# Kernel optimization log

Measured on AMD Instinct MI355X. Metric: run time of the kernel, lower is better.

Reference implementation:

```python
import jax, jax.numpy as jnp
import numpy as np

B, C, H, W = 2, 128, 64, 64
D_STATE, D_CONV, EXPAND = 16, 4, 2
D_INNER = EXPAND * C
DT_RANK = (C + 15) // 16  # ceil(d_model/16) = 8


def layernorm(x, w, b):
    # WithBias_LayerNorm over last (channel) dim, unbiased=False variance
    mu = jnp.mean(x, axis=-1, keepdims=True)
    var = jnp.mean((x - mu) ** 2, axis=-1, keepdims=True)
    return (x - mu) / jnp.sqrt(var + 1e-5) * w + b


def causal_conv1d_silu(x, w, b):
    # x: (b, d, l); w: (d, k) depthwise; causal pad k-1 on left, then SiLU
    k = w.shape[1]
    out = jax.lax.conv_general_dilated(
        x, w[:, None, :], window_strides=(1,), padding=[(k - 1, 0)],
        dimension_numbers=('NCH', 'OIH', 'NCH'), feature_group_count=w.shape[0])
    return jax.nn.silu(out + b[:, None])


def selective_scan(dA, dBu, Cm):
    # dA, dBu: (b, d, l, n); Cm: (b, n, l) -> y: (b, d, l)
    dA_t = jnp.moveaxis(dA, 2, 0)    # (l, b, d, n)
    dBu_t = jnp.moveaxis(dBu, 2, 0)  # (l, b, d, n)
    C_t = jnp.moveaxis(Cm, 2, 0)     # (l, b, n)

    def step(h, inp):
        a, bu, c = inp
        h = a * h + bu
        y = jnp.einsum('bdn,bn->bd', h, c)
        return h, y

    h0 = jnp.zeros(dA.shape[:2] + (dA.shape[3],), dA.dtype)
    _, ys = jax.lax.scan(step, h0, (dA_t, dBu_t, C_t))
    return jnp.moveaxis(ys, 0, 2)  # (b, d, l)


def mamba_branch(x3, W_in, W_z, conv_w, conv_b, W_x, W_dt, b_dt, A, D, W_out):
    # x3: (b, l, d_model) normalized input
    x = jnp.einsum('bld,ed->bel', x3, W_in)  # (b, d_inner, l)
    z = jnp.einsum('bld,ed->bel', x3, W_z)
    x = causal_conv1d_silu(x, conv_w, conv_b)
    xdbl = jnp.einsum('bdl,ed->bel', x, W_x)  # (b, dt_rank+2n, l)
    dt_low = xdbl[:, :DT_RANK]
    Bm = xdbl[:, DT_RANK:DT_RANK + D_STATE]
    Cm = xdbl[:, DT_RANK + D_STATE:]
    delta = jax.nn.softplus(jnp.einsum('brl,dr->bdl', dt_low, W_dt) + b_dt[:, None])
    dA = jnp.exp(delta[:, :, :, None] * A[None, :, None, :])           # (b,d,l,n)
    dBu = jnp.einsum('bdl,bnl->bdln', delta * x, Bm)                    # (b,d,l,n)
    y = selective_scan(dA, dBu, Cm)
    y = y + D[:, None] * x
    y = y * jax.nn.silu(z)
    return jnp.einsum('bdl,od->blo', y, W_out)  # (b, l, d_model)


def setup_inputs() -> dict:
    key = jax.random.key(0)
    ks = jax.random.split(key, 24)
    rn = lambda k, shp, s: jax.random.normal(k, shp, dtype=jnp.float32) * s
    inp = {}
    inp['pan'] = rn(ks[0], (B, C, H, W), 1.0)
    inp['ms'] = rn(ks[1], (B, C, H, W), 1.0)
    inp['norm_w_pan'] = jnp.ones((C,), jnp.float32)
    inp['norm_b_pan'] = jnp.zeros((C,), jnp.float32)
    inp['norm_w_ms'] = jnp.ones((C,), jnp.float32)
    inp['norm_b_ms'] = jnp.zeros((C,), jnp.float32)
    inp['W_in_pan'] = rn(ks[2], (D_INNER, C), C ** -0.5)
    inp['W_in_ms'] = rn(ks[3], (D_INNER, C), C ** -0.5)
    inp['W_z_pan'] = rn(ks[4], (D_INNER, C), C ** -0.5)
    inp['W_z_ms'] = rn(ks[5], (D_INNER, C), C ** -0.5)
    inp['conv_w_pan'] = rn(ks[6], (D_INNER, D_CONV), D_CONV ** -0.5)
    inp['conv_b_pan'] = rn(ks[7], (D_INNER,), 0.02)
    inp['conv_w_ms'] = rn(ks[8], (D_INNER, D_CONV), D_CONV ** -0.5)
    inp['conv_b_ms'] = rn(ks[9], (D_INNER,), 0.02)
    inp['W_x_pan'] = rn(ks[10], (DT_RANK + 2 * D_STATE, D_INNER), D_INNER ** -0.5)
    inp['W_x_ms'] = rn(ks[11], (DT_RANK + 2 * D_STATE, D_INNER), D_INNER ** -0.5)
    dt_std = DT_RANK ** -0.5
    inp['W_dt_pan'] = jax.random.uniform(ks[12], (D_INNER, DT_RANK), jnp.float32, -dt_std, dt_std)
    inp['W_dt_ms'] = jax.random.uniform(ks[13], (D_INNER, DT_RANK), jnp.float32, -dt_std, dt_std)
    # dt bias init: inverse-softplus of dt ~ logU[1e-3, 1e-1]
    u = np.asarray(jax.random.uniform(ks[14], (D_INNER,)))
    dt = np.exp(u * (np.log(0.1) - np.log(0.001)) + np.log(0.001)).clip(min=1e-4)
    inv_dt = dt + np.log(-np.expm1(-dt))
    inp['b_dt_pan'] = jnp.asarray(inv_dt, jnp.float32)
    inp['b_dt_ms'] = jnp.asarray(inv_dt, jnp.float32)
    inp['A_log'] = jnp.log(jnp.broadcast_to(jnp.arange(1, D_STATE + 1, dtype=jnp.float32), (D_INNER, D_STATE)))
    inp['D_pan'] = jnp.ones((D_INNER,), jnp.float32)
    inp['D_ms'] = jnp.ones((D_INNER,), jnp.float32)
    inp['W_out_pan'] = rn(ks[15], (C, D_INNER), D_INNER ** -0.5)
    inp['W_out_ms'] = rn(ks[16], (C, D_INNER), D_INNER ** -0.5)
    return inp


def reference(pan, ms, norm_w_pan, norm_b_pan, norm_w_ms, norm_b_ms,
              W_in_pan, W_in_ms, W_z_pan, W_z_ms,
              conv_w_pan, conv_b_pan, conv_w_ms, conv_b_ms,
              W_x_pan, W_x_ms, W_dt_pan, W_dt_ms, b_dt_pan, b_dt_ms,
              A_log, D_pan, D_ms, W_out_pan, W_out_ms):
    b, c, h, w = pan.shape
    A = -jnp.exp(A_log)
    pan3 = layernorm(pan.reshape(b, c, h * w).transpose(0, 2, 1), norm_w_pan, norm_b_pan)
    ms3 = layernorm(ms.reshape(b, c, h * w).transpose(0, 2, 1), norm_w_ms, norm_b_ms)
    out_pan = mamba_branch(pan3, W_in_pan, W_z_pan, conv_w_pan, conv_b_pan,
                           W_x_pan, W_dt_pan, b_dt_pan, A, D_pan, W_out_pan)
    out_ms = mamba_branch(ms3, W_in_ms, W_z_ms, conv_w_ms, conv_b_ms,
                          W_x_ms, W_dt_ms, b_dt_ms, A, D_ms, W_out_ms)
    out_pan = out_pan.transpose(0, 2, 1).reshape(b, c, h, w)
    out_ms = out_ms.transpose(0, 2, 1).reshape(b, c, h, w)
    return (out_pan, out_ms)
```

## Files before the change

### kernel.cpp

```cpp
#include <hip/hip_runtime.h>
#include <hip/hip_bf16.h>

constexpr int BB = 2;
constexpr int CC = 128;
constexpr int LL = 4096;
constexpr int DI = 256;
constexpr int DS = 16;
constexpr int DR = 8;
constexpr int DX = 40;
constexpr int NZ = 2 * BB;
constexpr int CH = 8;
constexpr int NCH = LL / CH;
constexpr int SEG = 32;

typedef short bf16x8 __attribute__((ext_vector_type(8)));
typedef float f32x4 __attribute__((ext_vector_type(4)));
typedef float f32x2 __attribute__((ext_vector_type(2)));

__device__ __forceinline__ unsigned short f2bf(float x) {
    __hip_bfloat16 h = __float2bfloat16(x);
    return *(unsigned short*)&h;
}
__device__ __forceinline__ float bflo(unsigned u) { return __uint_as_float(u << 16); }
__device__ __forceinline__ float bfhi(unsigned u) { return __uint_as_float(u & 0xffff0000u); }
__device__ __forceinline__ float bfu(unsigned short u) { return __uint_as_float((unsigned)u << 16); }
__device__ __forceinline__ float fast_rcp(float x) { return __builtin_amdgcn_rcpf(x); }
__device__ __forceinline__ float siluf(float x) { return x * fast_rcp(1.f + __expf(-x)); }
__device__ __forceinline__ float softplusf(float x) {
    const float z = exp2f(x * 1.44269504f);
    return (x > 20.f) ? x : 0.69314718f * log2f(1.f + z);
}

__global__ __launch_bounds__(256) void prep_kernel(
    const float* __restrict__ pan, const float* __restrict__ ms,
    const float* __restrict__ wpan, const float* __restrict__ bpan,
    const float* __restrict__ wms, const float* __restrict__ bms,
    const float* __restrict__ Winp, const float* __restrict__ Winm,
    const float* __restrict__ Wzp, const float* __restrict__ Wzm,
    const float* __restrict__ Woutp, const float* __restrict__ Woutm,
    const float* __restrict__ Wxp, const float* __restrict__ Wxm,
    unsigned short* __restrict__ x3b, unsigned short* __restrict__ wb)
{
    const int bx = blockIdx.x;
    const int t = threadIdx.x;
    if (bx >= 256) {
        const int i = (bx - 256) * 256 + t;
        const float* src; int off;
        if (i < 32768)       { src = Winp;  off = i; }
        else if (i < 65536)  { src = Winm;  off = i - 32768; }
        else if (i < 98304)  { src = Wzp;   off = i - 65536; }
        else if (i < 131072) { src = Wzm;   off = i - 98304; }
        else if (i < 163840) { src = Woutp; off = i - 131072; }
        else if (i < 196608) { src = Woutm; off = i - 163840; }
        else if (i < 206848) { src = Wxp;   off = i - 196608; }
        else                 { src = Wxm;   off = i - 206848; }
        wb[i] = f2bf(src[off]);
        return;
    }
    const int zi = bx >> 6;
    const int br = zi >> 1, b = zi & 1;
    const float* inp = br ? ms : pan;
    const float* wp = br ? wms : wpan;
    const float* bp = br ? bms : bpan;
    const int l0 = (bx & 63) * 64;
    const int lo = t & 63, c4 = t >> 6;
    const float* base = inp + (size_t)b * CC * LL + l0 + lo;
    float vals[32];
    float s = 0.f, s2 = 0.f;
    #pragma unroll
    for (int i = 0; i < 32; i++) {
        const int c = c4 * 32 + i;
        const float v = base[(size_t)c * LL];
        vals[i] = v; s += v; s2 += v * v;
    }
    __shared__ float red[2][4][64];
    red[0][c4][lo] = s; red[1][c4][lo] = s2;
    __syncthreads();
    const float S  = red[0][0][lo] + red[0][1][lo] + red[0][2][lo] + red[0][3][lo];
    const float S2 = red[1][0][lo] + red[1][1][lo] + red[1][2][lo] + red[1][3][lo];
    const float mu = S * (1.f / CC);
    const float var = S2 * (1.f / CC) - mu * mu;
    const float rstd = rsqrtf(var + 1e-5f);
    unsigned short* out = x3b + (size_t)zi * CC * LL + l0 + lo;
    #pragma unroll
    for (int i = 0; i < 32; i++) {
        const int c = c4 * 32 + i;
        out[(size_t)c * LL] = f2bf((vals[i] - mu) * rstd * wp[c] + bp[c]);
    }
}

__global__ __launch_bounds__(256) void gemm_inz_mfma(
    const unsigned short* __restrict__ wb, const unsigned short* __restrict__ x3b,
    unsigned short* __restrict__ xpre16, unsigned short* __restrict__ zb16)
{
    const int zi = blockIdx.z;
    const int my = blockIdx.y;
    const unsigned short* WI = wb + (zi >= BB ? 32768 : 0);
    const unsigned short* WZ = WI + 65536;
    const int mbase = my * 64;
    const unsigned short* Xb = x3b + (size_t)zi * CC * LL;
    const int n0 = blockIdx.x * 64;
    const int t = threadIdx.x;
    const int w = t >> 6, ln = t & 63;
    const int nf = ln & 15, qb = ln >> 4;
    bf16x8 afragI[4], afragZ[4];
    const int mrow = mbase + w * 16 + nf;
    #pragma unroll
    for (int c = 0; c < 4; c++) {
        afragI[c] = *(const bf16x8*)(WI + (size_t)mrow * CC + c * 32 + qb * 8);
        afragZ[c] = *(const bf16x8*)(WZ + (size_t)mrow * CC + c * 32 + qb * 8);
    }
    __shared__ unsigned short Bs[64][40];
    unsigned* Bw = (unsigned*)Bs;
    f32x4 accI[4] = {}, accZ[4] = {};
    const int kp = t >> 4, n4 = (t & 15) * 4;
    ushort4 a0 = *(const ushort4*)(Xb + (size_t)(2 * kp) * LL + n0 + n4);
    ushort4 a1 = *(const ushort4*)(Xb + (size_t)(2 * kp + 1) * LL + n0 + n4);
    #pragma unroll
    for (int kc = 0; kc < 4; kc++) {
        if (kc) __syncthreads();
        Bw[(n4 + 0) * 20 + kp] = (unsigned)a0.x | ((unsigned)a1.x << 16);
        Bw[(n4 + 1) * 20 + kp] = (unsigned)a0.y | ((unsigned)a1.y << 16);
        Bw[(n4 + 2) * 20 + kp] = (unsigned)a0.z | ((unsigned)a1.z << 16);
        Bw[(n4 + 3) * 20 + kp] = (unsigned)a0.w | ((unsigned)a1.w << 16);
        __syncthreads();
        if (kc < 3) {
            a0 = *(const ushort4*)(Xb + (size_t)((kc + 1) * 32 + 2 * kp) * LL + n0 + n4);
            a1 = *(const ushort4*)(Xb + (size_t)((kc + 1) * 32 + 2 * kp + 1) * LL + n0 + n4);
        }
        #pragma unroll
        for (int ns = 0; ns < 4; ns++) {
            const bf16x8 bf = *(const bf16x8*)(&Bs[ns * 16 + nf][qb * 8]);
            accI[ns] = __builtin_amdgcn_mfma_f32_16x16x32_bf16(afragI[kc], bf, accI[ns], 0, 0, 0);
            accZ[ns] = __builtin_amdgcn_mfma_f32_16x16x32_bf16(afragZ[kc], bf, accZ[ns], 0, 0, 0);
        }
    }
    #pragma unroll
    for (int ns = 0; ns < 4; ns++)
        #pragma unroll
        for (int r = 0; r < 4; r++) {
            const int m = mbase + w * 16 + qb * 4 + r;
            xpre16[((size_t)zi * DI + m) * LL + n0 + ns * 16 + nf] = f2bf(accI[ns][r]);
            zb16  [((size_t)zi * DI + m) * LL + n0 + ns * 16 + nf] = f2bf(siluf(accZ[ns][r]));
        }
}

__global__ __launch_bounds__(256) void gemm_x_mfma(
    const unsigned short* __restrict__ wb, const unsigned short* __restrict__ xpre16,
    const float* __restrict__ cw0, const float* __restrict__ cb0,
    const float* __restrict__ cw1, const float* __restrict__ cb1,
    unsigned short* __restrict__ xc, unsigned short* __restrict__ xdbl16)
{
    const int zi = blockIdx.z;
    const unsigned short* W = wb + 196608 + (zi >= BB ? 10240 : 0);
    const float* cw = (zi >= BB) ? cw1 : cw0;
    const float* cb = (zi >= BB) ? cb1 : cb0;
    const unsigned short* Xb = xpre16 + (size_t)zi * DI * LL;
    unsigned short* xcb = xc + (size_t)zi * DI * LL;
    const int n0 = blockIdx.x * 64;
    const int t = threadIdx.x;
    const int w = t >> 6, ln = t & 63;
    const int nf = ln & 15, qb = ln >> 4;
    bf16x8 zfrag;
    #pragma unroll
    for (int j = 0; j < 8; j++) zfrag[j] = 0;
    bf16x8 afrag[8];
    const int mrow = w * 16 + nf;
    #pragma unroll
    for (int c = 0; c < 8; c++)
        afrag[c] = (mrow < DX) ? *(const bf16x8*)(W + (size_t)mrow * DI + c * 32 + qb * 8) : zfrag;
    __shared__ unsigned short Bs[64][40];
    unsigned* Bw = (unsigned*)Bs;
    f32x4 acc[4] = {};
    const int kp = t >> 4, n4 = (t & 15) * 4;
    const bool edge = (n0 + n4 == 0);
    ushort4 cur0, cur1, prv0, prv1;
    {
        const unsigned short* xp0 = Xb + (size_t)(2 * kp) * LL + n0 + n4;
        const unsigned short* xp1 = Xb + (size_t)(2 * kp + 1) * LL + n0 + n4;
        cur0 = *(const ushort4*)xp0; cur1 = *(const ushort4*)xp1;
        if (!edge) { prv0 = *(const ushort4*)(xp0 - 4); prv1 = *(const ushort4*)(xp1 - 4); }
        else { prv0 = ushort4{0,0,0,0}; prv1 = ushort4{0,0,0,0}; }
    }
    #pragma unroll
    for (int kc = 0; kc < 8; kc++) {
        ushort4 o[2];
        #pragma unroll
        for (int rr = 0; rr < 2; rr++) {
            const int e = kc * 32 + 2 * kp + rr;
            const ushort4 cur = rr ? cur1 : cur0;
            const ushort4 prv = rr ? prv1 : prv0;
            const float xm3 = bfu(prv.y), xm2 = bfu(prv.z), xm1 = bfu(prv.w);
            const float c0 = bfu(cur.x), c1 = bfu(cur.y);
            const float c2 = bfu(cur.z), c3 = bfu(cur.w);
            const float w0 = cw[e * 4 + 0], w1 = cw[e * 4 + 1];
            const float w2 = cw[e * 4 + 2], w3 = cw[e * 4 + 3];
            const float bias = cb[e];
            o[rr].x = f2bf(siluf(w0 * xm3 + w1 * xm2 + w2 * xm1 + w3 * c0 + bias));
            o[rr].y = f2bf(siluf(w0 * xm2 + w1 * xm1 + w2 * c0 + w3 * c1 + bias));
            o[rr].z = f2bf(siluf(w0 * xm1 + w1 * c0 + w2 * c1 + w3 * c2 + bias));
            o[rr].w = f2bf(siluf(w0 * c0 + w1 * c1 + w2 * c2 + w3 * c3 + bias));
        }
        *(ushort4*)(xcb + (size_t)(kc * 32 + 2 * kp) * LL + n0 + n4) = o[0];
        *(ushort4*)(xcb + (size_t)(kc * 32 + 2 * kp + 1) * LL + n0 + n4) = o[1];
        if (kc) __syncthreads();
        Bw[(n4 + 0) * 20 + kp] = (unsigned)(unsigned short)o[0].x | ((unsigned)(unsigned short)o[1].x << 16);
        Bw[(n4 + 1) * 20 + kp] = (unsigned)(unsigned short)o[0].y | ((unsigned)(unsigned short)o[1].y << 16);
        Bw[(n4 + 2) * 20 + kp] = (unsigned)(unsigned short)o[0].z | ((unsigned)(unsigned short)o[1].z << 16);
        Bw[(n4 + 3) * 20 + kp] = (unsigned)(unsigned short)o[0].w | ((unsigned)(unsigned short)o[1].w << 16);
        __syncthreads();
        if (kc < 7) {
            const unsigned short* xp0 = Xb + (size_t)((kc + 1) * 32 + 2 * kp) * LL + n0 + n4;
            const unsigned short* xp1 = Xb + (size_t)((kc + 1) * 32 + 2 * kp + 1) * LL + n0 + n4;
            cur0 = *(const ushort4*)xp0; cur1 = *(const ushort4*)xp1;
            if (!edge) { prv0 = *(const ushort4*)(xp0 - 4); prv1 = *(const ushort4*)(xp1 - 4); }
        }
        #pragma unroll
        for (int ns = 0; ns < 4; ns++) {
            const bf16x8 bf = *(const bf16x8*)(&Bs[ns * 16 + nf][qb * 8]);
            acc[ns] = __builtin_amdgcn_mfma_f32_16x16x32_bf16(afrag[kc], bf, acc[ns], 0, 0, 0);
        }
    }
    #pragma unroll
    for (int ns = 0; ns < 4; ns++)
        #pragma unroll
        for (int r = 0; r < 4; r++) {
            const int m = w * 16 + qb * 4 + r;
            if (m < DX)
                xdbl16[((size_t)zi * DX + m) * LL + n0 + ns * 16 + nf] = f2bf(acc[ns][r]);
        }
}

__global__ __launch_bounds__(256) void gemm_out_mfma(
    const unsigned short* __restrict__ wb, const unsigned short* __restrict__ yb,
    float* __restrict__ outg)
{
    const int zi = blockIdx.z;
    const unsigned short* W = wb + 131072 + (zi >= BB ? 32768 : 0);
    const int mbase = blockIdx.y * 64;
    const unsigned short* Xb = yb + (size_t)zi * DI * LL;
    const int n0 = blockIdx.x * 64;
    const int t = threadIdx.x;
    const int w = t >> 6, ln = t & 63;
    const int nf = ln & 15, qb = ln >> 4;
    bf16x8 afrag[8];
    const int mrow = mbase + w * 16 + nf;
    #pragma unroll
    for (int c = 0; c < 8; c++)
        afrag[c] = *(const bf16x8*)(W + (size_t)mrow * DI + c * 32 + qb * 8);
    __shared__ unsigned short Bs[64][40];
    unsigned* Bw = (unsigned*)Bs;
    f32x4 acc[4] = {};
    const int kp = t >> 4, n4 = (t & 15) * 4;
    ushort4 a0 = *(const ushort4*)(Xb + (size_t)(2 * kp) * LL + n0 + n4);
    ushort4 a1 = *(const ushort4*)(Xb + (size_t)(2 * kp + 1) * LL + n0 + n4);
    #pragma unroll
    for (int kc = 0; kc < 8; kc++) {
        if (kc) __syncthreads();
        Bw[(n4 + 0) * 20 + kp] = (unsigned)a0.x | ((unsigned)a1.x << 16);
        Bw[(n4 + 1) * 20 + kp] = (unsigned)a0.y | ((unsigned)a1.y << 16);
        Bw[(n4 + 2) * 20 + kp] = (unsigned)a0.z | ((unsigned)a1.z << 16);
        Bw[(n4 + 3) * 20 + kp] = (unsigned)a0.w | ((unsigned)a1.w << 16);
        __syncthreads();
        if (kc < 7) {
            a0 = *(const ushort4*)(Xb + (size_t)((kc + 1) * 32 + 2 * kp) * LL + n0 + n4);
            a1 = *(const ushort4*)(Xb + (size_t)((kc + 1) * 32 + 2 * kp + 1) * LL + n0 + n4);
        }
        #pragma unroll
        for (int ns = 0; ns < 4; ns++) {
            const bf16x8 bf = *(const bf16x8*)(&Bs[ns * 16 + nf][qb * 8]);
            acc[ns] = __builtin_amdgcn_mfma_f32_16x16x32_bf16(afrag[kc], bf, acc[ns], 0, 0, 0);
        }
    }
    #pragma unroll
    for (int ns = 0; ns < 4; ns++)
        #pragma unroll
        for (int r = 0; r < 4; r++) {
            const int m = mbase + w * 16 + qb * 4 + r;
            outg[((size_t)zi * CC + m) * LL + n0 + ns * 16 + nf] = acc[ns][r];
        }
}

__global__ __launch_bounds__(512, 8) void scan_fused(
    const unsigned short* __restrict__ xc, const unsigned short* __restrict__ xdbl16,
    const float* __restrict__ A_log,
    const float* __restrict__ Wdt0, const float* __restrict__ Wdt1,
    const float* __restrict__ bdt0, const float* __restrict__ bdt1,
    const float* __restrict__ D0, const float* __restrict__ D1,
    const unsigned short* __restrict__ zb16, unsigned short* __restrict__ yb)
{
    const int blk = blockIdx.x;
    const int zi = blk >> 8;
    const int d  = blk & (DI - 1);
    const int t = threadIdx.x;
    const int l0 = t * CH;
    __shared__ float Ssh[DS * (NCH + 1)];
    __shared__ float sdl_sh[NCH];
    __shared__ float Pseg[DS * (SEG + 1)];
    __shared__ float Sseg[DS * (SEG + 1)];
    const unsigned short* xdb = xdbl16 + (size_t)zi * DX * LL;
    const float* Wdt = (zi >= BB) ? Wdt1 : Wdt0;
    const float* bdt = (zi >= BB) ? bdt1 : bdt0;
    const float dbias = bdt[d];
    float rx[CH];
    {
        const uint4 xv4 = *(const uint4*)(xc + (size_t)blk * LL + l0);
        rx[0] = bflo(xv4.x); rx[1] = bfhi(xv4.x);
        rx[2] = bflo(xv4.y); rx[3] = bfhi(xv4.y);
        rx[4] = bflo(xv4.z); rx[5] = bfhi(xv4.z);
        rx[6] = bflo(xv4.w); rx[7] = bfhi(xv4.w);
    }
    float e[CH], rdlx[CH];
    {
        f32x2 acc2[4];
        #pragma unroll
        for (int j = 0; j < 4; j++) acc2[j] = f32x2{dbias, dbias};
        #pragma unroll
        for (int r = 0; r < DR; r++) {
            const float wr = Wdt[d * DR + r];
            const f32x2 w2 = {wr, wr};
            const uint4 v = *(const uint4*)(xdb + (size_t)r * LL + l0);
            acc2[0] = w2 * f32x2{bflo(v.x), bfhi(v.x)} + acc2[0];
            acc2[1] = w2 * f32x2{bflo(v.y), bfhi(v.y)} + acc2[1];
            acc2[2] = w2 * f32x2{bflo(v.z), bfhi(v.z)} + acc2[2];
            acc2[3] = w2 * f32x2{bflo(v.w), bfhi(v.w)} + acc2[3];
        }
        float av[CH];
        av[0] = acc2[0].x; av[1] = acc2[0].y; av[2] = acc2[1].x; av[3] = acc2[1].y;
        av[4] = acc2[2].x; av[5] = acc2[2].y; av[6] = acc2[3].x; av[7] = acc2[3].y;
        float sdl = 0.f;
        #pragma unroll
        for (int i = 0; i < CH; i++) {
            const float sp = softplusf(av[i]);
            sdl += sp;
            rdlx[i] = sp * rx[i];
            e[i] = __expf(-sp);
        }
        sdl_sh[t] = sdl;
    }
    bool fast = true;
    #pragma unroll
    for (int n = 0; n < DS; n++)
        fast = fast && (fabsf(__expf(A_log[d * DS + n]) - (float)(n + 1)) < 1e-3f);
    const unsigned short* Bbase = xdb + (size_t)DR * LL;
    const unsigned short* Cbase = Bbase + (size_t)DS * LL;
    float y[CH];
    const int n2 = t & 15, sg = t >> 4;

    if (fast) {
        f32x2 e2[4], rdlx2[4];
        #pragma unroll
        for (int j = 0; j < 4; j++) {
            e2[j] = f32x2{e[2 * j], e[2 * j + 1]};
            rdlx2[j] = f32x2{rdlx[2 * j], rdlx[2 * j + 1]};
        }
        f32x2 pw2[4];
        #pragma unroll
        for (int j = 0; j < 4; j++) pw2[j] = f32x2{1.f, 1.f};
        #pragma unroll 4
        for (int n = 0; n < DS; n++) {
            const uint4 bv = *(const uint4*)(Bbase + (size_t)n * LL + l0);
            const f32x2 b0 = {bflo(bv.x), bfhi(bv.x)};
            const f32x2 b1 = {bflo(bv.y), bfhi(bv.y)};
            const f32x2 b2 = {bflo(bv.z), bfhi(bv.z)};
            const f32x2 b3 = {bflo(bv.w), bfhi(bv.w)};
            pw2[0] *= e2[0]; pw2[1] *= e2[1]; pw2[2] *= e2[2]; pw2[3] *= e2[3];
            const f32x2 u0 = rdlx2[0] * b0, u1 = rdlx2[1] * b1;
            const f32x2 u2 = rdlx2[2] * b2, u3 = rdlx2[3] * b3;
            float hn = u0.x;
            hn = fmaf(pw2[0].y, hn, u0.y);
            hn = fmaf(pw2[1].x, hn, u1.x);
            hn = fmaf(pw2[1].y, hn, u1.y);
            hn = fmaf(pw2[2].x, hn, u2.x);
            hn = fmaf(pw2[2].y, hn, u2.y);
            hn = fmaf(pw2[3].x, hn, u3.x);
            hn = fmaf(pw2[3].y, hn, u3.y);
            Ssh[n * (NCH + 1) + t] = hn;
        }
        __syncthreads();
        {
            const float Ann = -(float)(n2 + 1);
            float P = 1.f, S = 0.f;
            #pragma unroll
            for (int k = 0; k < 16; k++) {
                const int c = sg * 16 + k;
                const float p = __expf(Ann * sdl_sh[c]);
                const float s = Ssh[n2 * (NCH + 1) + c];
                S = fmaf(p, S, s);
                P *= p;
            }
            Pseg[n2 * (SEG + 1) + sg] = P;
            Sseg[n2 * (SEG + 1) + sg] = S;
        }
        __syncthreads();
        if (t < DS) {
            float h = 0.f;
            #pragma unroll 4
            for (int c2 = 0; c2 < SEG; c2++) {
                const float p = Pseg[t * (SEG + 1) + c2];
                const float s = Sseg[t * (SEG + 1) + c2];
                Sseg[t * (SEG + 1) + c2] = h;
                h = fmaf(p, h, s);
            }
        }
        __syncthreads();
        {
            const float Ann = -(float)(n2 + 1);
            float h = Sseg[n2 * (SEG + 1) + sg];
            #pragma unroll
            for (int k = 0; k < 16; k++) {
                const int c = sg * 16 + k;
                const float p = __expf(Ann * sdl_sh[c]);
                const float s = Ssh[n2 * (NCH + 1) + c];
                Ssh[n2 * (NCH + 1) + c] = h;
                h = fmaf(p, h, s);
            }
        }
        __syncthreads();
        f32x2 y2[4];
        #pragma unroll
        for (int j = 0; j < 4; j++) { y2[j] = f32x2{0.f, 0.f}; pw2[j] = f32x2{1.f, 1.f}; }
        #pragma unroll 2
        for (int n = 0; n < DS; n++) {
            const uint4 bv = *(const uint4*)(Bbase + (size_t)n * LL + l0);
            const uint4 cv = *(const uint4*)(Cbase + (size_t)n * LL + l0);
            const f32x2 b0 = {bflo(bv.x), bfhi(bv.x)};
            const f32x2 b1 = {bflo(bv.y), bfhi(bv.y)};
            const f32x2 b2 = {bflo(bv.z), bfhi(bv.z)};
            const f32x2 b3 = {bflo(bv.w), bfhi(bv.w)};
            const f32x2 c0 = {bflo(cv.x), bfhi(cv.x)};
            const f32x2 c1 = {bflo(cv.y), bfhi(cv.y)};
            const f32x2 c2 = {bflo(cv.z), bfhi(cv.z)};
            const f32x2 c3 = {bflo(cv.w), bfhi(cv.w)};
            pw2[0] *= e2[0]; pw2[1] *= e2[1]; pw2[2] *= e2[2]; pw2[3] *= e2[3];
            const f32x2 u0 = rdlx2[0] * b0, u1 = rdlx2[1] * b1;
            const f32x2 u2 = rdlx2[2] * b2, u3 = rdlx2[3] * b3;
            const float hp = Ssh[n * (NCH + 1) + t];
            const float h0 = fmaf(pw2[0].x, hp, u0.x);
            const float h1 = fmaf(pw2[0].y, h0, u0.y);
            y2[0] = f32x2{h0, h1} * c0 + y2[0];
            const float h2 = fmaf(pw2[1].x, h1, u1.x);
            const float h3 = fmaf(pw2[1].y, h2, u1.y);
            y2[1] = f32x2{h2, h3} * c1 + y2[1];
            const float h4 = fmaf(pw2[2].x, h3, u2.x);
            const float h5 = fmaf(pw2[2].y, h4, u2.y);
            y2[2] = f32x2{h4, h5} * c2 + y2[2];
            const float h6 = fmaf(pw2[3].x, h5, u3.x);
            const float h7 = fmaf(pw2[3].y, h6, u3.y);
            y2[3] = f32x2{h6, h7} * c3 + y2[3];
        }
        y[0] = y2[0].x; y[1] = y2[0].y; y[2] = y2[1].x; y[3] = y2[1].y;
        y[4] = y2[2].x; y[5] = y2[2].y; y[6] = y2[3].x; y[7] = y2[3].y;
    } else {
        float rdl[CH];
        #pragma unroll
        for (int i = 0; i < CH; i++) rdl[i] = -0.69314718f * log2f(e[i]);
        #pragma unroll 2
        for (int n = 0; n < DS; n++) {
            const float An = -__expf(A_log[d * DS + n]);
            const uint4 bv = *(const uint4*)(Bbase + (size_t)n * LL + l0);
            float hn = 0.f;
            hn = fmaf(__expf(rdl[0] * An), hn, rdlx[0] * bflo(bv.x));
            hn = fmaf(__expf(rdl[1] * An), hn, rdlx[1] * bfhi(bv.x));
            hn = fmaf(__expf(rdl[2] * An), hn, rdlx[2] * bflo(bv.y));
            hn = fmaf(__expf(rdl[3] * An), hn, rdlx[3] * bfhi(bv.y));
            hn = fmaf(__expf(rdl[4] * An), hn, rdlx[4] * bflo(bv.z));
            hn = fmaf(__expf(rdl[5] * An), hn, rdlx[5] * bfhi(bv.z));
            hn = fmaf(__expf(rdl[6] * An), hn, rdlx[6] * bflo(bv.w));
            hn = fmaf(__expf(rdl[7] * An), hn, rdlx[7] * bfhi(bv.w));
            Ssh[n * (NCH + 1) + t] = hn;
        }
        __syncthreads();
        {
            const float Ann = -__expf(A_log[d * DS + n2]);
            float P = 1.f, S = 0.f;
            #pragma unroll
            for (int k = 0; k < 16; k++) {
                const int c = sg * 16 + k;
                const float p = __expf(Ann * sdl_sh[c]);
                const float s = Ssh[n2 * (NCH + 1) + c];
                S = fmaf(p, S, s);
                P *= p;
            }
            Pseg[n2 * (SEG + 1) + sg] = P;
            Sseg[n2 * (SEG + 1) + sg] = S;
        }
        __syncthreads();
        if (t < DS) {
            float h = 0.f;
            #pragma unroll 4
            for (int c2 = 0; c2 < SEG; c2++) {
                const float p = Pseg[t * (SEG + 1) + c2];
                const float s = Sseg[t * (SEG + 1) + c2];
                Sseg[t * (SEG + 1) + c2] = h;
                h = fmaf(p, h, s);
            }
        }
        __syncthreads();
        {
            const float Ann = -__expf(A_log[d * DS + n2]);
            float h = Sseg[n2 * (SEG + 1) + sg];
            #pragma unroll
            for (int k = 0; k < 16; k++) {
                const int c = sg * 16 + k;
                const float p = __expf(Ann * sdl_sh[c]);
                const float s = Ssh[n2 * (NCH + 1) + c];
                Ssh[n2 * (NCH + 1) + c] = h;
                h = fmaf(p, h, s);
            }
        }
        __syncthreads();
        #pragma unroll
        for (int i = 0; i < CH; i++) y[i] = 0.f;
        #pragma unroll 2
        for (int n = 0; n < DS; n++) {
            const float An = -__expf(A_log[d * DS + n]);
            const uint4 bv = *(const uint4*)(Bbase + (size_t)n * LL + l0);
            const uint4 cv = *(const uint4*)(Cbase + (size_t)n * LL + l0);
            float hn = Ssh[n * (NCH + 1) + t];
            hn = fmaf(__expf(rdl[0] * An), hn, rdlx[0] * bflo(bv.x)); y[0] = fmaf(hn, bflo(cv.x), y[0]);
            hn = fmaf(__expf(rdl[1] * An), hn, rdlx[1] * bfhi(bv.x)); y[1] = fmaf(hn, bfhi(cv.x), y[1]);
            hn = fmaf(__expf(rdl[2] * An), hn, rdlx[2] * bflo(bv.y)); y[2] = fmaf(hn, bflo(cv.y), y[2]);
            hn = fmaf(__expf(rdl[3] * An), hn, rdlx[3] * bfhi(bv.y)); y[3] = fmaf(hn, bfhi(bv.y), y[3]);
            hn = fmaf(__expf(rdl[4] * An), hn, rdlx[4] * bflo(bv.z)); y[4] = fmaf(hn, bflo(cv.z), y[4]);
            hn = fmaf(__expf(rdl[5] * An), hn, rdlx[5] * bfhi(bv.z)); y[5] = fmaf(hn, bfhi(cv.z), y[5]);
            hn = fmaf(__expf(rdl[6] * An), hn, rdlx[6] * bflo(bv.w)); y[6] = fmaf(hn, bflo(cv.w), y[6]);
            hn = fmaf(__expf(rdl[7] * An), hn, rdlx[7] * bfhi(cv.w)); y[7] = fmaf(hn, bfhi(cv.w), y[7]);
        }
    }
    const float Dd = ((zi >= BB) ? D1 : D0)[d];
    const unsigned short* z_g = zb16 + (size_t)blk * LL + l0;
    unsigned short* y_g = yb + (size_t)blk * LL + l0;
    {
        const uint4 zv = *(const uint4*)z_g;
        float zf[CH];
        zf[0] = bflo(zv.x); zf[1] = bfhi(zv.x); zf[2] = bflo(zv.y); zf[3] = bfhi(zv.y);
        zf[4] = bflo(zv.z); zf[5] = bfhi(zv.z); zf[6] = bflo(zv.w); zf[7] = bfhi(zv.w);
        ushort4 r0, r1;
        #pragma unroll
        for (int i = 0; i < CH; i++) {
            const float val = (y[i] + Dd * rx[i]) * zf[i];
            if (i < 4) ((unsigned short*)&r0)[i] = f2bf(val);
            else       ((unsigned short*)&r1)[i - 4] = f2bf(val);
        }
        *(ushort4*)(y_g + 0) = r0;
        *(ushort4*)(y_g + 4) = r1;
    }
}

extern "C" void kernel_launch(void* const* d_in, const int* in_sizes, int n_in,
                              void* d_out, int out_size, void* d_ws, size_t ws_size,
                              hipStream_t stream)
{
    (void)in_sizes; (void)n_in; (void)out_size; (void)ws_size;
    auto fp = [&](int i) { return (const float*)d_in[i]; };
    const float *pan = fp(0), *ms = fp(1);
    const float *nwp = fp(2), *nbp = fp(3), *nwm = fp(4), *nbm = fp(5);
    const float *Winp = fp(6), *Winm = fp(7), *Wzp = fp(8), *Wzm = fp(9);
    const float *cwp = fp(10), *cbp = fp(11), *cwm = fp(12), *cbm = fp(13);
    const float *Wxp = fp(14), *Wxm = fp(15);
    const float *Wdtp = fp(16), *Wdtm = fp(17), *bdtp = fp(18), *bdtm = fp(19);
    const float *Alog = fp(20), *Dp = fp(21), *Dm = fp(22);
    const float *Woutp = fp(23), *Woutm = fp(24);

    unsigned short* us = (unsigned short*)d_ws;
    unsigned short* x3b    = us;
    unsigned short* xpre16 = x3b    + (size_t)NZ * CC * LL;
    unsigned short* zb16   = xpre16 + (size_t)NZ * DI * LL;
    unsigned short* xdbl16 = zb16   + (size_t)NZ * DI * LL;
    unsigned short* yb     = xdbl16 + (size_t)NZ * DX * LL;
    unsigned short* xc     = yb     + (size_t)NZ * DI * LL;
    unsigned short* wb     = xc     + (size_t)NZ * DI * LL;
    float* out = (float*)d_out;

    prep_kernel<<<dim3(256 + 848), 256, 0, stream>>>(
        pan, ms, nwp, nbp, nwm, nbm,
        Winp, Winm, Wzp, Wzm, Woutp, Woutm, Wxp, Wxm, x3b, wb);
    gemm_inz_mfma<<<dim3(LL / 64, 4, NZ), 256, 0, stream>>>(wb, x3b, xpre16, zb16);
    gemm_x_mfma<<<dim3(LL / 64, 1, NZ), 256, 0, stream>>>(wb, xpre16, cwp, cbp, cwm, cbm, xc, xdbl16);
    scan_fused<<<dim3(NZ * DI), 512, 0, stream>>>(xc, xdbl16, Alog, Wdtp, Wdtm, bdtp, bdtm,
                                                  Dp, Dm, zb16, yb);
    gemm_out_mfma<<<dim3(LL / 64, 2, NZ), 256, 0, stream>>>(wb, yb, out);
}
```

Measured before the change: 169.2 us.

## Split x_proj GEMM K dimension across two blocks and add combine kernel

The conv+x_proj kernel now splits its 256-wide reduction into two halves on a new grid y dimension, doubling the block count from 256 to 512. Each half writes fp32 partial sums to a new workspace buffer, and a separate combine kernel adds them and converts to bf16. The goal is better CU occupancy for a small-grid kernel, paid for with an extra launch and extra fp32 traffic. The diff also fixes two wrong B/C operand indices in the scan inner loop.

```diff
diff --git a/kernel.cpp b/kernel.cpp
--- a/kernel.cpp
+++ b/kernel.cpp
@@ -149,9 +149,10 @@
     const unsigned short* __restrict__ wb, const unsigned short* __restrict__ xpre16,
     const float* __restrict__ cw0, const float* __restrict__ cb0,
     const float* __restrict__ cw1, const float* __restrict__ cb1,
-    unsigned short* __restrict__ xc, unsigned short* __restrict__ xdbl16)
+    unsigned short* __restrict__ xc, float* __restrict__ xpart)
 {
     const int zi = blockIdx.z;
+    const int h = blockIdx.y;
     const unsigned short* W = wb + 196608 + (zi >= BB ? 10240 : 0);
     const float* cw = (zi >= BB) ? cw1 : cw0;
     const float* cb = (zi >= BB) ? cb1 : cb0;
@@ -164,30 +165,31 @@
     bf16x8 zfrag;
     #pragma unroll
     for (int j = 0; j < 8; j++) zfrag[j] = 0;
-    bf16x8 afrag[8];
+    bf16x8 afrag[4];
     const int mrow = w * 16 + nf;
     #pragma unroll
-    for (int c = 0; c < 8; c++)
-        afrag[c] = (mrow < DX) ? *(const bf16x8*)(W + (size_t)mrow * DI + c * 32 + qb * 8) : zfrag;
+    for (int c = 0; c < 4; c++)
+        afrag[c] = (mrow < DX) ? *(const bf16x8*)(W + (size_t)mrow * DI + (4 * h + c) * 32 + qb * 8) : zfrag;
     __shared__ unsigned short Bs[64][40];
     unsigned* Bw = (unsigned*)Bs;
     f32x4 acc[4] = {};
     const int kp = t >> 4, n4 = (t & 15) * 4;
     const bool edge = (n0 + n4 == 0);
+    const int rbase = h * 128;
     ushort4 cur0, cur1, prv0, prv1;
     {
-        const unsigned short* xp0 = Xb + (size_t)(2 * kp) * LL + n0 + n4;
-        const unsigned short* xp1 = Xb + (size_t)(2 * kp + 1) * LL + n0 + n4;
+        const unsigned short* xp0 = Xb + (size_t)(rbase + 2 * kp) * LL + n0 + n4;
+        const unsigned short* xp1 = Xb + (size_t)(rbase + 2 * kp + 1) * LL + n0 + n4;
         cur0 = *(const ushort4*)xp0; cur1 = *(const ushort4*)xp1;
         if (!edge) { prv0 = *(const ushort4*)(xp0 - 4); prv1 = *(const ushort4*)(xp1 - 4); }
         else { prv0 = ushort4{0,0,0,0}; prv1 = ushort4{0,0,0,0}; }
     }
     #pragma unroll
-    for (int kc = 0; kc < 8; kc++) {
+    for (int kc = 0; kc < 4; kc++) {
         ushort4 o[2];
         #pragma unroll
         for (int rr = 0; rr < 2; rr++) {
-            const int e = kc * 32 + 2 * kp + rr;
+            const int e = rbase + kc * 32 + 2 * kp + rr;
             const ushort4 cur = rr ? cur1 : cur0;
             const ushort4 prv = rr ? prv1 : prv0;
             const float xm3 = bfu(prv.y), xm2 = bfu(prv.z), xm1 = bfu(prv.w);
@@ -201,17 +203,17 @@
             o[rr].z = f2bf(siluf(w0 * xm1 + w1 * c0 + w2 * c1 + w3 * c2 + bias));
             o[rr].w = f2bf(siluf(w0 * c0 + w1 * c1 + w2 * c2 + w3 * c3 + bias));
         }
-        *(ushort4*)(xcb + (size_t)(kc * 32 + 2 * kp) * LL + n0 + n4) = o[0];
-        *(ushort4*)(xcb + (size_t)(kc * 32 + 2 * kp + 1) * LL + n0 + n4) = o[1];
+        *(ushort4*)(xcb + (size_t)(rbase + kc * 32 + 2 * kp) * LL + n0 + n4) = o[0];
+        *(ushort4*)(xcb + (size_t)(rbase + kc * 32 + 2 * kp + 1) * LL + n0 + n4) = o[1];
         if (kc) __syncthreads();
         Bw[(n4 + 0) * 20 + kp] = (unsigned)(unsigned short)o[0].x | ((unsigned)(unsigned short)o[1].x << 16);
         Bw[(n4 + 1) * 20 + kp] = (unsigned)(unsigned short)o[0].y | ((unsigned)(unsigned short)o[1].y << 16);
         Bw[(n4 + 2) * 20 + kp] = (unsigned)(unsigned short)o[0].z | ((unsigned)(unsigned short)o[1].z << 16);
         Bw[(n4 + 3) * 20 + kp] = (unsigned)(unsigned short)o[0].w | ((unsigned)(unsigned short)o[1].w << 16);
         __syncthreads();
-        if (kc < 7) {
-            const unsigned short* xp0 = Xb + (size_t)((kc + 1) * 32 + 2 * kp) * LL + n0 + n4;
-            const unsigned short* xp1 = Xb + (size_t)((kc + 1) * 32 + 2 * kp + 1) * LL + n0 + n4;
+        if (kc < 3) {
+            const unsigned short* xp0 = Xb + (size_t)(rbase + (kc + 1) * 32 + 2 * kp) * LL + n0 + n4;
+            const unsigned short* xp1 = Xb + (size_t)(rbase + (kc + 1) * 32 + 2 * kp + 1) * LL + n0 + n4;
             cur0 = *(const ushort4*)xp0; cur1 = *(const ushort4*)xp1;
             if (!edge) { prv0 = *(const ushort4*)(xp0 - 4); prv1 = *(const ushort4*)(xp1 - 4); }
         }
@@ -221,14 +223,27 @@
             acc[ns] = __builtin_amdgcn_mfma_f32_16x16x32_bf16(afrag[kc], bf, acc[ns], 0, 0, 0);
         }
     }
+    float* xp = xpart + (size_t)h * NZ * DX * LL;
     #pragma unroll
     for (int ns = 0; ns < 4; ns++)
         #pragma unroll
         for (int r = 0; r < 4; r++) {
             const int m = w * 16 + qb * 4 + r;
             if (m < DX)
-                xdbl16[((size_t)zi * DX + m) * LL + n0 + ns * 16 + nf] = f2bf(acc[ns][r]);
-        }
+                xp[((size_t)zi * DX + m) * LL + n0 + ns * 16 + nf] = acc[ns][r];
+        }
+}
+
+__global__ __launch_bounds__(256) void combine_x(
+    const float* __restrict__ xpart, unsigned short* __restrict__ xdbl16)
+{
+    const int idx = blockIdx.x * 256 + threadIdx.x;
+    const float4 a = ((const float4*)xpart)[idx];
+    const float4 b = ((const float4*)(xpart + (size_t)NZ * DX * LL))[idx];
+    ushort4 o;
+    o.x = f2bf(a.x + b.x); o.y = f2bf(a.y + b.y);
+    o.z = f2bf(a.z + b.z); o.w = f2bf(a.w + b.w);
+    ((ushort4*)xdbl16)[idx] = o;
 }
 
 __global__ __launch_bounds__(256) void gemm_out_mfma(
@@ -521,11 +536,11 @@
             hn = fmaf(__expf(rdl[0] * An), hn, rdlx[0] * bflo(bv.x)); y[0] = fmaf(hn, bflo(cv.x), y[0]);
             hn = fmaf(__expf(rdl[1] * An), hn, rdlx[1] * bfhi(bv.x)); y[1] = fmaf(hn, bfhi(cv.x), y[1]);
             hn = fmaf(__expf(rdl[2] * An), hn, rdlx[2] * bflo(bv.y)); y[2] = fmaf(hn, bflo(cv.y), y[2]);
-            hn = fmaf(__expf(rdl[3] * An), hn, rdlx[3] * bfhi(bv.y)); y[3] = fmaf(hn, bfhi(bv.y), y[3]);
+            hn = fmaf(__expf(rdl[3] * An), hn, rdlx[3] * bfhi(bv.y)); y[3] = fmaf(hn, bfhi(cv.y), y[3]);
             hn = fmaf(__expf(rdl[4] * An), hn, rdlx[4] * bflo(bv.z)); y[4] = fmaf(hn, bflo(cv.z), y[4]);
             hn = fmaf(__expf(rdl[5] * An), hn, rdlx[5] * bfhi(bv.z)); y[5] = fmaf(hn, bfhi(cv.z), y[5]);
             hn = fmaf(__expf(rdl[6] * An), hn, rdlx[6] * bflo(bv.w)); y[6] = fmaf(hn, bflo(cv.w), y[6]);
-            hn = fmaf(__expf(rdl[7] * An), hn, rdlx[7] * bfhi(cv.w)); y[7] = fmaf(hn, bfhi(cv.w), y[7]);
+            hn = fmaf(__expf(rdl[7] * An), hn, rdlx[7] * bfhi(bv.w)); y[7] = fmaf(hn, bfhi(cv.w), y[7]);
         }
     }
     const float Dd = ((zi >= BB) ? D1 : D0)[d];
@@ -571,13 +586,15 @@
     unsigned short* yb     = xdbl16 + (size_t)NZ * DX * LL;
     unsigned short* xc     = yb     + (size_t)NZ * DI * LL;
     unsigned short* wb     = xc     + (size_t)NZ * DI * LL;
+    float* xpart = (float*)(wb + 217088 + 512);
     float* out = (float*)d_out;
 
     prep_kernel<<<dim3(256 + 848), 256, 0, stream>>>(
         pan, ms, nwp, nbp, nwm, nbm,
         Winp, Winm, Wzp, Wzm, Woutp, Woutm, Wxp, Wxm, x3b, wb);
     gemm_inz_mfma<<<dim3(LL / 64, 4, NZ), 256, 0, stream>>>(wb, x3b, xpre16, zb16);
-    gemm_x_mfma<<<dim3(LL / 64, 1, NZ), 256, 0, stream>>>(wb, xpre16, cwp, cbp, cwm, cbm, xc, xdbl16);
+    gemm_x_mfma<<<dim3(LL / 64, 2, NZ), 256, 0, stream>>>(wb, xpre16, cwp, cbp, cwm, cbm, xc, xpart);
+    combine_x<<<dim3(NZ * DX * LL / 4 / 256), 256, 0, stream>>>(xpart, xdbl16);
     scan_fused<<<dim3(NZ * DI), 512, 0, stream>>>(xc, xdbl16, Alog, Wdtp, Wdtm, bdtp, bdtm,
                                                   Dp, Dm, zb16, yb);
     gemm_out_mfma<<<dim3(LL / 64, 2, NZ), 256, 0, stream>>>(wb, yb, out);
```

After: 170.3 us. About the same (+0.7%).

## Fuse local chunk scan with output pass, add carry-in correction via decay powers

Applied to the files above, without the earlier changes.

The fast path now computes the zero-initialised local chunk recurrence and its C-weighted output in a single pass, storing each chunk's final state for the cross-chunk scan. Afterwards it adds the carry-in contribution as h_in times the cumulative decay power times C, so B no longer has to be read a second time and the serial recurrence no longer has to be recomputed. It also fixes two swapped bv/cv operands in the slow fallback path. The cost is an extra pass over C with extra multiplies for the cumulative decay powers per state.

```diff
diff --git a/kernel.cpp b/kernel.cpp
--- a/kernel.cpp
+++ b/kernel.cpp
@@ -354,72 +354,9 @@
             e2[j] = f32x2{e[2 * j], e[2 * j + 1]};
             rdlx2[j] = f32x2{rdlx[2 * j], rdlx[2 * j + 1]};
         }
-        f32x2 pw2[4];
-        #pragma unroll
-        for (int j = 0; j < 4; j++) pw2[j] = f32x2{1.f, 1.f};
-        #pragma unroll 4
-        for (int n = 0; n < DS; n++) {
-            const uint4 bv = *(const uint4*)(Bbase + (size_t)n * LL + l0);
-            const f32x2 b0 = {bflo(bv.x), bfhi(bv.x)};
-            const f32x2 b1 = {bflo(bv.y), bfhi(bv.y)};
-            const f32x2 b2 = {bflo(bv.z), bfhi(bv.z)};
-            const f32x2 b3 = {bflo(bv.w), bfhi(bv.w)};
-            pw2[0] *= e2[0]; pw2[1] *= e2[1]; pw2[2] *= e2[2]; pw2[3] *= e2[3];
-            const f32x2 u0 = rdlx2[0] * b0, u1 = rdlx2[1] * b1;
-            const f32x2 u2 = rdlx2[2] * b2, u3 = rdlx2[3] * b3;
-            float hn = u0.x;
-            hn = fmaf(pw2[0].y, hn, u0.y);
-            hn = fmaf(pw2[1].x, hn, u1.x);
-            hn = fmaf(pw2[1].y, hn, u1.y);
-            hn = fmaf(pw2[2].x, hn, u2.x);
-            hn = fmaf(pw2[2].y, hn, u2.y);
-            hn = fmaf(pw2[3].x, hn, u3.x);
-            hn = fmaf(pw2[3].y, hn, u3.y);
-            Ssh[n * (NCH + 1) + t] = hn;
-        }
-        __syncthreads();
-        {
-            const float Ann = -(float)(n2 + 1);
-            float P = 1.f, S = 0.f;
-            #pragma unroll
-            for (int k = 0; k < 16; k++) {
-                const int c = sg * 16 + k;
-                const float p = __expf(Ann * sdl_sh[c]);
-                const float s = Ssh[n2 * (NCH + 1) + c];
-                S = fmaf(p, S, s);
-                P *= p;
-            }
-            Pseg[n2 * (SEG + 1) + sg] = P;
-            Sseg[n2 * (SEG + 1) + sg] = S;
-        }
-        __syncthreads();
-        if (t < DS) {
-            float h = 0.f;
-            #pragma unroll 4
-            for (int c2 = 0; c2 < SEG; c2++) {
-                const float p = Pseg[t * (SEG + 1) + c2];
-                const float s = Sseg[t * (SEG + 1) + c2];
-                Sseg[t * (SEG + 1) + c2] = h;
-                h = fmaf(p, h, s);
-            }
-        }
-        __syncthreads();
-        {
-            const float Ann = -(float)(n2 + 1);
-            float h = Sseg[n2 * (SEG + 1) + sg];
-            #pragma unroll
-            for (int k = 0; k < 16; k++) {
-                const int c = sg * 16 + k;
-                const float p = __expf(Ann * sdl_sh[c]);
-                const float s = Ssh[n2 * (NCH + 1) + c];
-                Ssh[n2 * (NCH + 1) + c] = h;
-                h = fmaf(p, h, s);
-            }
-        }
-        __syncthreads();
-        f32x2 y2[4];
-        #pragma unroll
-        for (int j = 0; j < 4; j++) { y2[j] = f32x2{0.f, 0.f}; pw2[j] = f32x2{1.f, 1.f}; }
+        f32x2 pw2[4], y2[4];
+        #pragma unroll
+        for (int j = 0; j < 4; j++) { pw2[j] = f32x2{1.f, 1.f}; y2[j] = f32x2{0.f, 0.f}; }
         #pragma unroll 2
         for (int n = 0; n < DS; n++) {
             const uint4 bv = *(const uint4*)(Bbase + (size_t)n * LL + l0);
@@ -435,8 +372,7 @@
             pw2[0] *= e2[0]; pw2[1] *= e2[1]; pw2[2] *= e2[2]; pw2[3] *= e2[3];
             const f32x2 u0 = rdlx2[0] * b0, u1 = rdlx2[1] * b1;
             const f32x2 u2 = rdlx2[2] * b2, u3 = rdlx2[3] * b3;
-            const float hp = Ssh[n * (NCH + 1) + t];
-            const float h0 = fmaf(pw2[0].x, hp, u0.x);
+            const float h0 = u0.x;
             const float h1 = fmaf(pw2[0].y, h0, u0.y);
             y2[0] = f32x2{h0, h1} * c0 + y2[0];
             const float h2 = fmaf(pw2[1].x, h1, u1.x);
@@ -448,6 +384,78 @@
             const float h6 = fmaf(pw2[3].x, h5, u3.x);
             const float h7 = fmaf(pw2[3].y, h6, u3.y);
             y2[3] = f32x2{h6, h7} * c3 + y2[3];
+            Ssh[n * (NCH + 1) + t] = h7;
+        }
+        f32x2 p2[4];
+        {
+            const float P0 = e2[0].x;
+            const float P1 = P0 * e2[0].y;
+            const float P2 = P1 * e2[1].x;
+            const float P3 = P2 * e2[1].y;
+            const float P4 = P3 * e2[2].x;
+            const float P5 = P4 * e2[2].y;
+            const float P6 = P5 * e2[3].x;
+            const float P7 = P6 * e2[3].y;
+            p2[0] = f32x2{P0, P1}; p2[1] = f32x2{P2, P3};
+            p2[2] = f32x2{P4, P5}; p2[3] = f32x2{P6, P7};
+        }
+        __syncthreads();
+        {
+            const float Ann = -(float)(n2 + 1);
+            float P = 1.f, S = 0.f;
+            #pragma unroll
+            for (int k = 0; k < 16; k++) {
+                const int c = sg * 16 + k;
+                const float p = __expf(Ann * sdl_sh[c]);
+                const float s = Ssh[n2 * (NCH + 1) + c];
+                S = fmaf(p, S, s);
+                P *= p;
+            }
+            Pseg[n2 * (SEG + 1) + sg] = P;
+            Sseg[n2 * (SEG + 1) + sg] = S;
+        }
+        __syncthreads();
+        if (t < DS) {
+            float h = 0.f;
+            #pragma unroll 4
+            for (int c2 = 0; c2 < SEG; c2++) {
+                const float p = Pseg[t * (SEG + 1) + c2];
+                const float s = Sseg[t * (SEG + 1) + c2];
+                Sseg[t * (SEG + 1) + c2] = h;
+                h = fmaf(p, h, s);
+            }
+        }
+        __syncthreads();
+        {
+            const float Ann = -(float)(n2 + 1);
+            float h = Sseg[n2 * (SEG + 1) + sg];
+            #pragma unroll
+            for (int k = 0; k < 16; k++) {
+                const int c = sg * 16 + k;
+                const float p = __expf(Ann * sdl_sh[c]);
+                const float s = Ssh[n2 * (NCH + 1) + c];
+                Ssh[n2 * (NCH + 1) + c] = h;
+                h = fmaf(p, h, s);
+            }
+        }
+        __syncthreads();
+        f32x2 cp2[4];
+        #pragma unroll
+        for (int j = 0; j < 4; j++) cp2[j] = f32x2{1.f, 1.f};
+        #pragma unroll 4
+        for (int n = 0; n < DS; n++) {
+            const uint4 cv = *(const uint4*)(Cbase + (size_t)n * LL + l0);
+            const f32x2 c0 = {bflo(cv.x), bfhi(cv.x)};
+            const f32x2 c1 = {bflo(cv.y), bfhi(cv.y)};
+            const f32x2 c2 = {bflo(cv.z), bfhi(cv.z)};
+            const f32x2 c3 = {bflo(cv.w), bfhi(cv.w)};
+            cp2[0] *= p2[0]; cp2[1] *= p2[1]; cp2[2] *= p2[2]; cp2[3] *= p2[3];
+            const float h = Ssh[n * (NCH + 1) + t];
+            const f32x2 hh = {h, h};
+            y2[0] = (cp2[0] * hh) * c0 + y2[0];
+            y2[1] = (cp2[1] * hh) * c1 + y2[1];
+            y2[2] = (cp2[2] * hh) * c2 + y2[2];
+            y2[3] = (cp2[3] * hh) * c3 + y2[3];
         }
         y[0] = y2[0].x; y[1] = y2[0].y; y[2] = y2[1].x; y[3] = y2[1].y;
         y[4] = y2[2].x; y[5] = y2[2].y; y[6] = y2[3].x; y[7] = y2[3].y;
@@ -521,11 +529,11 @@
             hn = fmaf(__expf(rdl[0] * An), hn, rdlx[0] * bflo(bv.x)); y[0] = fmaf(hn, bflo(cv.x), y[0]);
             hn = fmaf(__expf(rdl[1] * An), hn, rdlx[1] * bfhi(bv.x)); y[1] = fmaf(hn, bfhi(cv.x), y[1]);
             hn = fmaf(__expf(rdl[2] * An), hn, rdlx[2] * bflo(bv.y)); y[2] = fmaf(hn, bflo(cv.y), y[2]);
-            hn = fmaf(__expf(rdl[3] * An), hn, rdlx[3] * bfhi(bv.y)); y[3] = fmaf(hn, bfhi(bv.y), y[3]);
+            hn = fmaf(__expf(rdl[3] * An), hn, rdlx[3] * bfhi(bv.y)); y[3] = fmaf(hn, bfhi(cv.y), y[3]);
             hn = fmaf(__expf(rdl[4] * An), hn, rdlx[4] * bflo(bv.z)); y[4] = fmaf(hn, bflo(cv.z), y[4]);
             hn = fmaf(__expf(rdl[5] * An), hn, rdlx[5] * bfhi(bv.z)); y[5] = fmaf(hn, bfhi(cv.z), y[5]);
             hn = fmaf(__expf(rdl[6] * An), hn, rdlx[6] * bflo(bv.w)); y[6] = fmaf(hn, bflo(cv.w), y[6]);
-            hn = fmaf(__expf(rdl[7] * An), hn, rdlx[7] * bfhi(cv.w)); y[7] = fmaf(hn, bfhi(cv.w), y[7]);
+            hn = fmaf(__expf(rdl[7] * An), hn, rdlx[7] * bfhi(bv.w)); y[7] = fmaf(hn, bfhi(cv.w), y[7]);
         }
     }
     const float Dd = ((zi >= BB) ? D1 : D0)[d];
```

After: 167.7 us. About the same (-0.8%).
